# Performance work log

Hardware: AMD Instinct MI355X
Metric: run time of the kernel (lower is better)

The kernel has to match this reference:

```python
import math
import jax, jax.numpy as jnp
import numpy as np

DIM = 1024
N_HEADS = 16
HEAD_DIM = DIM // N_HEADS
MAX_SEQ_LEN = 4096
ROPE_BASE = 10000.0


def _rope_tables(seq_len):
    # [S, head_dim//2] cos/sin tables, matching RotaryPositionalEncoding buffers
    inv_freq = 1.0 / (ROPE_BASE ** (jnp.arange(0, HEAD_DIM, 2, dtype=jnp.float32) / HEAD_DIM))
    t = jnp.arange(seq_len, dtype=jnp.float32)
    freqs = jnp.outer(t, inv_freq)
    return jnp.cos(freqs), jnp.sin(freqs)


def _rotate_half(x):
    # interleaved rotate: out[..., 0::2] = -x[..., 1::2]; out[..., 1::2] = x[..., 0::2]
    x1 = x[..., 0::2]
    x2 = x[..., 1::2]
    return jnp.stack([-x2, x1], axis=-1).reshape(x.shape)


def _apply_rope(xq, xk, cos, sin):
    # cos/sin: [S, head_dim//2] -> repeat_interleave(2) -> [1, 1, S, head_dim]
    cos = jnp.repeat(cos, 2, axis=-1)[None, None]
    sin = jnp.repeat(sin, 2, axis=-1)[None, None]
    xq_out = xq * cos + _rotate_half(xq) * sin
    xk_out = xk * cos + _rotate_half(xk) * sin
    return xq_out, xk_out


def setup_inputs() -> dict:
    key = jax.random.key(0)
    kx, kq, kk, kv, ko = jax.random.split(key, 5)
    B, S = 1, 4096
    x = jax.random.normal(kx, (B, S, DIM), dtype=jnp.float32)
    scale = 0.02
    Wq = jax.random.normal(kq, (DIM, DIM), dtype=jnp.float32) * scale
    Wk = jax.random.normal(kk, (DIM, DIM), dtype=jnp.float32) * scale
    Wv = jax.random.normal(kv, (DIM, DIM), dtype=jnp.float32) * scale
    Wo = jax.random.normal(ko, (DIM, DIM), dtype=jnp.float32) * scale
    return {"x": x, "Wq": Wq, "Wk": Wk, "Wv": Wv, "Wo": Wo}


def reference(x, Wq, Wk, Wv, Wo):
    B, S, _ = x.shape
    # torch nn.Linear: y = x @ W.T
    q = (x @ Wq.T).reshape(B, S, N_HEADS, HEAD_DIM).transpose(0, 2, 1, 3)  # [B,H,S,D]
    k = (x @ Wk.T).reshape(B, S, N_HEADS, HEAD_DIM).transpose(0, 2, 1, 3)
    v = (x @ Wv.T).reshape(B, S, N_HEADS, HEAD_DIM).transpose(0, 2, 1, 3)

    cos, sin = _rope_tables(S)  # start_pos = 0
    q, k = _apply_rope(q, k, cos, sin)

    scores = jnp.einsum('bhqd,bhkd->bhqk', q, k) / math.sqrt(HEAD_DIM)
    # causal mask (start_pos=0, no KV cache): upper triangle above diag gets -inf
    mask = jnp.triu(jnp.full((S, S), -jnp.inf, dtype=scores.dtype), k=1)
    scores = scores + mask[None, None]
    probs = jax.nn.softmax(scores, axis=-1)
    out = jnp.einsum('bhqk,bhkd->bhqd', probs, v)  # [B,H,S,D]
    out = out.transpose(0, 2, 1, 3).reshape(B, S, DIM)
    return out @ Wo.T
```

## Files before the change

kernel.cpp:

```cpp
#include <hip/hip_runtime.h>


typedef __attribute__((ext_vector_type(4))) float f32x4;
typedef __attribute__((ext_vector_type(8))) short short8;
typedef __attribute__((ext_vector_type(2))) unsigned int u32x2;
typedef unsigned short u16;

#define SEQ 4096
#define DIMM 1024
#define NH 16
#define HD 64

__device__ __forceinline__ u16 f2b(float f) {
  unsigned u = __float_as_uint(f);
  u += 0x7FFFu + ((u >> 16) & 1u);
  return (u16)(u >> 16);
}
__device__ __forceinline__ f32x4 mfma16(short8 a, short8 b, f32x4 c) {
  return __builtin_amdgcn_mfma_f32_16x16x32_bf16(a, b, c, 0, 0, 0);
}
#define GLL16(gp, lp)                                                        \
  __builtin_amdgcn_global_load_lds(                                          \
      (const __attribute__((address_space(1))) unsigned int*)(gp),           \
      (__attribute__((address_space(3))) unsigned int*)(lp), 16, 0, 0)

__global__ __launch_bounds__(256) void cvt_all(
    const float* __restrict__ x, const float* __restrict__ wq,
    const float* __restrict__ wk, const float* __restrict__ wv,
    const float* __restrict__ wo,
    u16* __restrict__ xb, u16* __restrict__ wqb, u16* __restrict__ wkb,
    u16* __restrict__ wvb, u16* __restrict__ wob, float2* __restrict__ tab) {
  int i = blockIdx.x * 256 + threadIdx.x;
  if (i < 2097152) {
    const float* src;
    u16* dst;
    int j;
    if (i < 1048576) {
      src = x; dst = xb; j = i;
    } else {
      int t = i - 1048576;
      int wsel = t >> 18;
      j = t & 262143;
      src = (wsel == 0) ? wq : (wsel == 1) ? wk : (wsel == 2) ? wv : wo;
      dst = (wsel == 0) ? wqb : (wsel == 1) ? wkb : (wsel == 2) ? wvb : wob;
    }
    float4 v = ((const float4*)src)[j];
    ushort4 o;
    o.x = f2b(v.x); o.y = f2b(v.y); o.z = f2b(v.z); o.w = f2b(v.w);
    ((ushort4*)dst)[j] = o;
  } else {
    int j = i - 2097152;
    int s = j >> 6, d = j & 63, fi = d >> 1;
    float ang = (float)s * powf(10000.0f, -(float)fi * (1.0f / 32.0f));
    float sn, cs;
    sincosf(ang, &sn, &cs);
    tab[j] = make_float2(cs, (d & 1) ? sn : -sn);
  }
}

__global__ __launch_bounds__(256) void gemm_qkv(
    const u16* __restrict__ A, const u16* __restrict__ B,
    const float2* __restrict__ tab, u16* __restrict__ Qh, u16* __restrict__ Kh,
    u16* __restrict__ Vh) {
  const int K = DIMM;
  __shared__ __align__(16) u16 As[2][4096];
  __shared__ __align__(16) u16 Bs[2][4096];
  const int tid = threadIdx.x;
  const int bm = blockIdx.x, bn = blockIdx.y;
  const int w = tid >> 6, lane = tid & 63;
  const int wm = w >> 1, wn = w & 1;
  const int l15 = lane & 15, g = lane >> 4;

  f32x4 acc[4][4] = {};

  const u16* Ap0 = A + (size_t)(bm * 128 + (tid >> 2)) * K + (tid & 3) * 8;
  const u16* Ap1 = Ap0 + (size_t)64 * K;
  const u16* Bp0 = B + (size_t)(bn * 128 + (tid >> 2)) * K + (tid & 3) * 8;
  const u16* Bp1 = Bp0 + (size_t)64 * K;

  GLL16(Ap0, &As[0][w * 512]);
  GLL16(Ap1, &As[0][2048 + w * 512]);
  GLL16(Bp0, &Bs[0][w * 512]);
  GLL16(Bp1, &Bs[0][2048 + w * 512]);
  __syncthreads();

  const int nk = K >> 5;
  for (int t = 0; t < nk; ++t) {
    const int cur = t & 1;
    if (t + 1 < nk) {
      const int k1 = (t + 1) * 32;
      GLL16(Ap0 + k1, &As[cur ^ 1][w * 512]);
      GLL16(Ap1 + k1, &As[cur ^ 1][2048 + w * 512]);
      GLL16(Bp0 + k1, &Bs[cur ^ 1][w * 512]);
      GLL16(Bp1 + k1, &Bs[cur ^ 1][2048 + w * 512]);
    }
    short8 af[4], bf[4];
#pragma unroll
    for (int m = 0; m < 4; ++m)
      af[m] = *(const short8*)&As[cur][(wm * 64 + m * 16 + l15) * 32 + g * 8];
#pragma unroll
    for (int n = 0; n < 4; ++n)
      bf[n] = *(const short8*)&Bs[cur][(wn * 64 + n * 16 + l15) * 32 + g * 8];
#pragma unroll
    for (int m = 0; m < 4; ++m)
#pragma unroll
      for (int n = 0; n < 4; ++n)
        acc[m][n] = mfma16(af[m], bf[n], acc[m][n]);
    __syncthreads();
  }

  const int sector = bn >> 3;
  const int hh = (bn & 7) * 2 + wn;
  u16* dst = (sector == 0) ? Qh : (sector == 1) ? Kh : Vh;
  const float qs = (sector == 0) ? 0.125f : 1.0f;
  const int evenlane = !(l15 & 1);
  const int dd0 = (l15 & ~1);
#pragma unroll
  for (int m = 0; m < 4; ++m) {
    const int sb = bm * 128 + wm * 64 + m * 16 + g * 4;
#pragma unroll
    for (int n = 0; n < 4; ++n) {
      const int d = n * 16 + l15;
      float val[4];
#pragma unroll
      for (int r = 0; r < 4; ++r) {
        float v = acc[m][n][r];
        if (sector < 2) {
          float p = __shfl_xor(v, 1);
          float2 tc = tab[(sb + r) * 64 + d];
          val[r] = (v * tc.x + p * tc.y) * qs;
        } else {
          val[r] = v;
        }
      }
      float x0 = __shfl_xor(val[0], 1);
      float x1 = __shfl_xor(val[1], 1);
      float x2 = __shfl_xor(val[2], 1);
      float x3 = __shfl_xor(val[3], 1);
      float aLo = evenlane ? val[0] : x2;
      float aHi = evenlane ? x0 : val[2];
      float bLo = evenlane ? val[1] : x3;
      float bHi = evenlane ? x1 : val[3];
      unsigned pkA, pkB;
      asm("v_cvt_pk_bf16_f32 %0, %1, %2" : "=v"(pkA) : "v"(aLo), "v"(aHi));
      asm("v_cvt_pk_bf16_f32 %0, %1, %2" : "=v"(pkB) : "v"(bLo), "v"(bHi));
      const int rA = evenlane ? 0 : 2, rB = evenlane ? 1 : 3;
      const int dcol = n * 16 + dd0;
      *(unsigned*)&dst[((size_t)hh * SEQ + sb + rA) * HD + dcol] = pkA;
      *(unsigned*)&dst[((size_t)hh * SEQ + sb + rB) * HD + dcol] = pkB;
    }
  }
}

__global__ __launch_bounds__(256) void gemm_o(
    const u16* __restrict__ A, const u16* __restrict__ B, float* __restrict__ C) {
  const int K = DIMM;
  __shared__ __align__(16) u16 As[2][4096];
  __shared__ __align__(16) u16 Bs[2][2048];
  const int tid = threadIdx.x;
  const int bm = blockIdx.x, bn = blockIdx.y;
  const int w = tid >> 6, lane = tid & 63;
  const int wm = w >> 1, wn = w & 1;
  const int l15 = lane & 15, g = lane >> 4;

  f32x4 acc[4][2] = {};

  const u16* Ap0 = A + (size_t)(bm * 128 + (tid >> 2)) * K + (tid & 3) * 8;
  const u16* Ap1 = Ap0 + (size_t)64 * K;
  const u16* Bp0 = B + (size_t)(bn * 64 + (tid >> 2)) * K + (tid & 3) * 8;

  GLL16(Ap0, &As[0][w * 512]);
  GLL16(Ap1, &As[0][2048 + w * 512]);
  GLL16(Bp0, &Bs[0][w * 512]);
  __syncthreads();

  const int nk = K >> 5;
  for (int t = 0; t < nk; ++t) {
    const int cur = t & 1;
    if (t + 1 < nk) {
      const int k1 = (t + 1) * 32;
      GLL16(Ap0 + k1, &As[cur ^ 1][w * 512]);
      GLL16(Ap1 + k1, &As[cur ^ 1][2048 + w * 512]);
      GLL16(Bp0 + k1, &Bs[cur ^ 1][w * 512]);
    }
    short8 af[4], bf[2];
#pragma unroll
    for (int m = 0; m < 4; ++m)
      af[m] = *(const short8*)&As[cur][(wm * 64 + m * 16 + l15) * 32 + g * 8];
#pragma unroll
    for (int n = 0; n < 2; ++n)
      bf[n] = *(const short8*)&Bs[cur][(wn * 32 + n * 16 + l15) * 32 + g * 8];
#pragma unroll
    for (int m = 0; m < 4; ++m)
#pragma unroll
      for (int n = 0; n < 2; ++n)
        acc[m][n] = mfma16(af[m], bf[n], acc[m][n]);
    __syncthreads();
  }

#pragma unroll
  for (int m = 0; m < 4; ++m) {
    int grow = bm * 128 + wm * 64 + m * 16 + g * 4;
#pragma unroll
    for (int n = 0; n < 2; ++n) {
      int gcol = bn * 64 + wn * 32 + n * 16 + l15;
#pragma unroll
      for (int r = 0; r < 4; ++r)
        C[(size_t)(grow + r) * DIMM + gcol] = acc[m][n][r];
    }
  }
}

__global__ __launch_bounds__(256, 4) void attn_fwd(
    const u16* __restrict__ Qh, const u16* __restrict__ Kh,
    const u16* __restrict__ Vh, u16* __restrict__ Ob,
    float* __restrict__ Opart, float2* __restrict__ ml) {
  __shared__ __align__(16) u16 Ks[2][64 * 64];
  __shared__ __align__(16) u16 Vt[2][64 * 64];
  __shared__ __align__(16) u16 Ps[4][16 * 64];

  const int L = blockIdx.x;
  const int h = L & 15;
  const int u = L >> 4;
  int c, t0, t1, half = 0;
  if (u < 80) {
    int i = u / 5, j = u % 5;
    if (j < 4) {
      c = 63 - 2 * i - (j >> 1);
      half = j & 1;
      int mid = (c + 2) >> 1;
      t0 = half ? mid : 0;
      t1 = half ? (c + 1) : mid;
    } else {
      c = 31 - i; t0 = 0; t1 = c + 1;
    }
  } else {
    c = 15 - (u - 80); t0 = 0; t1 = c + 1;
  }
  const int heavy = (c >= 32);
  const int nt = t1 - t0;

  const int tid = threadIdx.x, w = tid >> 6, lane = tid & 63;
  const int l15 = lane & 15, g = lane >> 4;
  const int qr0 = c * 64 + w * 16;
  const size_t hS = (size_t)h * SEQ;

  const int krow0 = w * 8 + (lane >> 3);
  const int kc0 = ((lane & 7) ^ (krow0 & 7)) * 8;
  const int krow1 = 32 + krow0;
  const int kc1 = ((lane & 7) ^ (krow1 & 7)) * 8;
  const int kvp = tid >> 3, d0 = (tid & 7) * 8;
  const u16* Vsrc = Vh + (hS + kvp * 2) * HD + d0;
  int voff[8];
#pragma unroll
  for (int j = 0; j < 8; ++j) {
    int d = d0 + j;
    int sw = (d ^ (d >> 3)) & 7;
    voff[j] = d * 64 + (((kvp >> 2) ^ sw) << 3) + (kvp & 3) * 2;
  }

  const u16* Qp = Qh + (hS + qr0 + l15) * HD + g * 8;
  short8 qf0 = *(const short8*)(Qp);
  short8 qf1 = *(const short8*)(Qp + 32);

  f32x4 o[4] = {};
  float m_ = -3.0e38f, lg = 0.f;

  GLL16(Kh + (hS + (size_t)t0 * 64 + krow0) * HD + kc0, &Ks[0][w * 512]);
  GLL16(Kh + (hS + (size_t)t0 * 64 + krow1) * HD + kc1, &Ks[0][2048 + w * 512]);
  short8 va = *(const short8*)(Vsrc + (size_t)t0 * 64 * HD);
  short8 vb = *(const short8*)(Vsrc + (size_t)t0 * 64 * HD + HD);

  for (int tt = 0; tt < nt; ++tt) {
    const int t = t0 + tt;
    const int cur = tt & 1;
    {
      u16* vtb = &Vt[cur][0];
#pragma unroll
      for (int j = 0; j < 8; ++j) {
        ushort2 pr;
        pr.x = (u16)va[j];
        pr.y = (u16)vb[j];
        *(ushort2*)(vtb + voff[j]) = pr;
      }
    }
    __syncthreads();
    if (tt + 1 < nt) {
      const size_t kb_ = hS + (size_t)(t + 1) * 64;
      GLL16(Kh + (kb_ + krow0) * HD + kc0, &Ks[cur ^ 1][w * 512]);
      GLL16(Kh + (kb_ + krow1) * HD + kc1, &Ks[cur ^ 1][2048 + w * 512]);
      va = *(const short8*)(Vsrc + (size_t)(t + 1) * 64 * HD);
      vb = *(const short8*)(Vsrc + (size_t)(t + 1) * 64 * HD + HD);
    }
    f32x4 s[4] = {};
    __builtin_amdgcn_s_setprio(1);
#pragma unroll
    for (int kb = 0; kb < 4; ++kb) {
      int row = kb * 16 + l15;
      short8 k0 = *(const short8*)&Ks[cur][row * 64 + ((g ^ (row & 7)) << 3)];
      short8 k1 = *(const short8*)&Ks[cur][row * 64 + (((4 + g) ^ (row & 7)) << 3)];
      s[kb] = mfma16(k0, qf0, s[kb]);
      s[kb] = mfma16(k1, qf1, s[kb]);
    }
    __builtin_amdgcn_s_setprio(0);
    if (t == c) {
      const int kv0 = t * 64;
      int q = qr0 + l15;
#pragma unroll
      for (int kb = 0; kb < 4; ++kb) {
        int kvb = kv0 + kb * 16 + g * 4;
#pragma unroll
        for (int r = 0; r < 4; ++r)
          if (kvb + r > q) s[kb][r] = -1.0e30f;
      }
    }
    float mx = fmaxf(fmaxf(fmaxf(s[0][0], s[0][1]), fmaxf(s[0][2], s[0][3])),
                     fmaxf(fmaxf(fmaxf(s[1][0], s[1][1]), fmaxf(s[1][2], s[1][3])),
                           fmaxf(fmaxf(fmaxf(s[2][0], s[2][1]), fmaxf(s[2][2], s[2][3])),
                                 fmaxf(fmaxf(s[3][0], s[3][1]), fmaxf(s[3][2], s[3][3])))));
    mx = fmaxf(mx, __shfl_xor(mx, 16));
    mx = fmaxf(mx, __shfl_xor(mx, 32));
    if (!__all(mx - m_ <= 8.0f)) {
      float nm = fmaxf(m_, mx);
      float sc = __expf(m_ - nm);
      m_ = nm;
      lg *= sc;
#pragma unroll
      for (int r = 0; r < 4; ++r) {
        float so = __shfl(sc, g * 4 + r);
        o[0][r] *= so; o[1][r] *= so; o[2][r] *= so; o[3][r] *= so;
      }
    }
    {
      float ps = 0.f;
#pragma unroll
      for (int kb = 0; kb < 4; ++kb) {
        float p0 = __expf(s[kb][0] - m_);
        float p1 = __expf(s[kb][1] - m_);
        float p2 = __expf(s[kb][2] - m_);
        float p3 = __expf(s[kb][3] - m_);
        ps += (p0 + p1) + (p2 + p3);
        unsigned w0, w1;
        asm("v_cvt_pk_bf16_f32 %0, %1, %2" : "=v"(w0) : "v"(p0), "v"(p1));
        asm("v_cvt_pk_bf16_f32 %0, %1, %2" : "=v"(w1) : "v"(p2), "v"(p3));
        int ch = (kb * 2 + (g >> 1)) ^ (l15 & 7);
        *(u32x2*)&Ps[w][l15 * 64 + ch * 8 + (g & 1) * 4] = (u32x2){w0, w1};
      }
      lg += ps;
    }
    short8 pa0 = *(const short8*)&Ps[w][l15 * 64 + ((g ^ (l15 & 7)) << 3)];
    short8 pa1 = *(const short8*)&Ps[w][l15 * 64 + (((4 + g) ^ (l15 & 7)) << 3)];
    __builtin_amdgcn_s_setprio(1);
#pragma unroll
    for (int nb = 0; nb < 4; ++nb) {
      int rv = nb * 16 + l15;
      int swv = (rv ^ (rv >> 3)) & 7;
      short8 v0f = *(const short8*)&Vt[cur][rv * 64 + ((g ^ swv) << 3)];
      short8 v1f = *(const short8*)&Vt[cur][rv * 64 + (((4 + g) ^ swv) << 3)];
      o[nb] = mfma16(pa0, v0f, o[nb]);
      o[nb] = mfma16(pa1, v1f, o[nb]);
    }
    __builtin_amdgcn_s_setprio(0);
  }

  float l = lg;
  l += __shfl_xor(l, 16);
  l += __shfl_xor(l, 32);
  if (heavy) {
    const int p = (h * 32 + (c - 32)) * 2 + half;
    if (lane < 16)
      ml[p * 64 + w * 16 + l15] = make_float2(m_, l);
    float* Od = Opart + ((size_t)p << 12);
#pragma unroll
    for (int nb = 0; nb < 4; ++nb)
#pragma unroll
      for (int r = 0; r < 4; ++r)
        Od[(w * 16 + g * 4 + r) * 64 + nb * 16 + l15] = o[nb][r];
  } else {
    float il = 1.0f / l;
#pragma unroll
    for (int r = 0; r < 4; ++r) {
      float ilr = __shfl(il, g * 4 + r);
      int qrow = qr0 + g * 4 + r;
#pragma unroll
      for (int nb = 0; nb < 4; ++nb)
        Ob[(size_t)qrow * DIMM + h * HD + nb * 16 + l15] = f2b(o[nb][r] * ilr);
    }
  }
}

__global__ __launch_bounds__(256) void attn_merge(
    const float* __restrict__ Opart, const float2* __restrict__ ml,
    u16* __restrict__ Ob) {
  const int slot = blockIdx.x;
  const int h = slot >> 5;
  const int c = 32 + (slot & 31);
  const int t = threadIdx.x;
  const int q = t >> 2, dq = (t & 3) << 4;
  const int pA = slot * 2, pB = pA + 1;
  float2 a = ml[pA * 64 + q], b = ml[pB * 64 + q];
  float m = fmaxf(a.x, b.x);
  float fA = __expf(a.x - m), fB = __expf(b.x - m);
  float il = 1.0f / (a.y * fA + b.y * fB);
  const float* OA = Opart + ((size_t)pA << 12) + q * 64 + dq;
  const float* OB = Opart + ((size_t)pB << 12) + q * 64 + dq;
  u16* dst = Ob + (size_t)(c * 64 + q) * DIMM + h * HD + dq;
#pragma unroll
  for (int jj = 0; jj < 16; jj += 4) {
    float4 va = *(const float4*)(OA + jj);
    float4 vb = *(const float4*)(OB + jj);
    ushort4 o4;
    o4.x = f2b((va.x * fA + vb.x * fB) * il);
    o4.y = f2b((va.y * fA + vb.y * fB) * il);
    o4.z = f2b((va.z * fA + vb.z * fB) * il);
    o4.w = f2b((va.w * fA + vb.w * fB) * il);
    *(ushort4*)(dst + jj) = o4;
  }
}

#define OFF_XB 0u
#define OFF_WQKV 8388608u
#define OFF_WOB 14680064u
#define OFF_TAB 16777216u
#define OFF_QH 18874368u
#define OFF_KH 27262976u
#define OFF_VH 35651584u
#define OFF_OB 44040192u
#define OFF_OPART 52428800u
#define OFF_ML 69206016u

extern "C" void kernel_launch(void* const* d_in, const int* in_sizes, int n_in,
                              void* d_out, int out_size, void* d_ws, size_t ws_size,
                              hipStream_t stream) {
  const float* x = (const float*)d_in[0];
  const float* Wq = (const float*)d_in[1];
  const float* Wk = (const float*)d_in[2];
  const float* Wv = (const float*)d_in[3];
  const float* Wo = (const float*)d_in[4];
  float* out = (float*)d_out;
  char* ws = (char*)d_ws;

  u16* xb = (u16*)(ws + OFF_XB);
  u16* wqkv = (u16*)(ws + OFF_WQKV);
  u16* wqb = wqkv;
  u16* wkb = wqkv + (size_t)DIMM * DIMM;
  u16* wvb = wqkv + (size_t)2 * DIMM * DIMM;
  u16* wob = (u16*)(ws + OFF_WOB);
  float2* tab = (float2*)(ws + OFF_TAB);
  u16* Qh = (u16*)(ws + OFF_QH);
  u16* Kh = (u16*)(ws + OFF_KH);
  u16* Vh = (u16*)(ws + OFF_VH);
  u16* Ob = (u16*)(ws + OFF_OB);
  float* Opart = (float*)(ws + OFF_OPART);
  float2* ml = (float2*)(ws + OFF_ML);

  cvt_all<<<9216, 256, 0, stream>>>(x, Wq, Wk, Wv, Wo, xb, wqb, wkb, wvb, wob, tab);

  gemm_qkv<<<dim3(32, 24), 256, 0, stream>>>(xb, wqkv, tab, Qh, Kh, Vh);

  attn_fwd<<<1536, 256, 0, stream>>>(Qh, Kh, Vh, Ob, Opart, ml);

  attn_merge<<<512, 256, 0, stream>>>(Opart, ml, Ob);

  gemm_o<<<dim3(32, 16), 256, 0, stream>>>(Ob, wob, out);
}
```

Measured before the change: 231.0 us.

## Pre-transpose V into a separate buffer and swizzle GEMM LDS tiles

Result: no change. 234.1 us (+1.3%).

```diff
diff --git a/kernel.cpp b/kernel.cpp
--- a/kernel.cpp
+++ b/kernel.cpp
@@ -73,9 +73,11 @@
 
   f32x4 acc[4][4] = {};
 
-  const u16* Ap0 = A + (size_t)(bm * 128 + (tid >> 2)) * K + (tid & 3) * 8;
+  const int arow = tid >> 2;
+  const int acol = ((tid & 3) ^ ((arow >> 1) & 3)) * 8;
+  const u16* Ap0 = A + (size_t)(bm * 128 + arow) * K + acol;
   const u16* Ap1 = Ap0 + (size_t)64 * K;
-  const u16* Bp0 = B + (size_t)(bn * 128 + (tid >> 2)) * K + (tid & 3) * 8;
+  const u16* Bp0 = B + (size_t)(bn * 128 + arow) * K + acol;
   const u16* Bp1 = Bp0 + (size_t)64 * K;
 
   GLL16(Ap0, &As[0][w * 512]);
@@ -84,6 +86,8 @@
   GLL16(Bp1, &Bs[0][2048 + w * 512]);
   __syncthreads();
 
+  const int kx = (l15 >> 1) & 3;
+  const int c0 = (g ^ kx) << 3;
   const int nk = K >> 5;
   for (int t = 0; t < nk; ++t) {
     const int cur = t & 1;
@@ -97,10 +101,10 @@
     short8 af[4], bf[4];
 #pragma unroll
     for (int m = 0; m < 4; ++m)
-      af[m] = *(const short8*)&As[cur][(wm * 64 + m * 16 + l15) * 32 + g * 8];
+      af[m] = *(const short8*)&As[cur][(wm * 64 + m * 16 + l15) * 32 + c0];
 #pragma unroll
     for (int n = 0; n < 4; ++n)
-      bf[n] = *(const short8*)&Bs[cur][(wn * 64 + n * 16 + l15) * 32 + g * 8];
+      bf[n] = *(const short8*)&Bs[cur][(wn * 64 + n * 16 + l15) * 32 + c0];
 #pragma unroll
     for (int m = 0; m < 4; ++m)
 #pragma unroll
@@ -152,6 +156,31 @@
   }
 }
 
+__global__ __launch_bounds__(256) void vtrans(
+    const u16* __restrict__ Vh, u16* __restrict__ VhT) {
+  __shared__ u16 T[64][72];
+  const int b = blockIdx.x;
+  const int h = b >> 6, s0 = (b & 63) * 64;
+  const int tid = threadIdx.x;
+  const int r = tid >> 3, c8 = (tid & 7) * 8;
+#pragma unroll
+  for (int rep = 0; rep < 2; ++rep) {
+    const int row = rep * 32 + r;
+    *(short8*)&T[row][c8] =
+        *(const short8*)&Vh[((size_t)h * SEQ + s0 + row) * HD + c8];
+  }
+  __syncthreads();
+  const int d = tid >> 2;
+#pragma unroll
+  for (int rep = 0; rep < 2; ++rep) {
+    const int ss = (tid & 3) * 8 + rep * 32;
+    short8 v;
+#pragma unroll
+    for (int j = 0; j < 8; ++j) v[j] = T[ss + j][d];
+    *(short8*)&VhT[((size_t)h * HD + d) * SEQ + s0 + ss] = v;
+  }
+}
+
 __global__ __launch_bounds__(256) void gemm_o(
     const u16* __restrict__ A, const u16* __restrict__ B, float* __restrict__ C) {
   const int K = DIMM;
@@ -165,15 +194,19 @@
 
   f32x4 acc[4][2] = {};
 
-  const u16* Ap0 = A + (size_t)(bm * 128 + (tid >> 2)) * K + (tid & 3) * 8;
+  const int arow = tid >> 2;
+  const int acol = ((tid & 3) ^ ((arow >> 1) & 3)) * 8;
+  const u16* Ap0 = A + (size_t)(bm * 128 + arow) * K + acol;
   const u16* Ap1 = Ap0 + (size_t)64 * K;
-  const u16* Bp0 = B + (size_t)(bn * 64 + (tid >> 2)) * K + (tid & 3) * 8;
+  const u16* Bp0 = B + (size_t)(bn * 64 + arow) * K + acol;
 
   GLL16(Ap0, &As[0][w * 512]);
   GLL16(Ap1, &As[0][2048 + w * 512]);
   GLL16(Bp0, &Bs[0][w * 512]);
   __syncthreads();
 
+  const int kx = (l15 >> 1) & 3;
+  const int c0 = (g ^ kx) << 3;
   const int nk = K >> 5;
   for (int t = 0; t < nk; ++t) {
     const int cur = t & 1;
@@ -186,10 +219,10 @@
     short8 af[4], bf[2];
 #pragma unroll
     for (int m = 0; m < 4; ++m)
-      af[m] = *(const short8*)&As[cur][(wm * 64 + m * 16 + l15) * 32 + g * 8];
+      af[m] = *(const short8*)&As[cur][(wm * 64 + m * 16 + l15) * 32 + c0];
 #pragma unroll
     for (int n = 0; n < 2; ++n)
-      bf[n] = *(const short8*)&Bs[cur][(wn * 32 + n * 16 + l15) * 32 + g * 8];
+      bf[n] = *(const short8*)&Bs[cur][(wn * 32 + n * 16 + l15) * 32 + c0];
 #pragma unroll
     for (int m = 0; m < 4; ++m)
 #pragma unroll
@@ -213,7 +246,7 @@
 
 __global__ __launch_bounds__(256, 4) void attn_fwd(
     const u16* __restrict__ Qh, const u16* __restrict__ Kh,
-    const u16* __restrict__ Vh, u16* __restrict__ Ob,
+    const u16* __restrict__ VhT, u16* __restrict__ Ob,
     float* __restrict__ Opart, float2* __restrict__ ml) {
   __shared__ __align__(16) u16 Ks[2][64 * 64];
   __shared__ __align__(16) u16 Vt[2][64 * 64];
@@ -244,20 +277,12 @@
   const int l15 = lane & 15, g = lane >> 4;
   const int qr0 = c * 64 + w * 16;
   const size_t hS = (size_t)h * SEQ;
+  const size_t hD = (size_t)h * HD;
 
   const int krow0 = w * 8 + (lane >> 3);
   const int kc0 = ((lane & 7) ^ (krow0 & 7)) * 8;
   const int krow1 = 32 + krow0;
   const int kc1 = ((lane & 7) ^ (krow1 & 7)) * 8;
-  const int kvp = tid >> 3, d0 = (tid & 7) * 8;
-  const u16* Vsrc = Vh + (hS + kvp * 2) * HD + d0;
-  int voff[8];
-#pragma unroll
-  for (int j = 0; j < 8; ++j) {
-    int d = d0 + j;
-    int sw = (d ^ (d >> 3)) & 7;
-    voff[j] = d * 64 + (((kvp >> 2) ^ sw) << 3) + (kvp & 3) * 2;
-  }
 
   const u16* Qp = Qh + (hS + qr0 + l15) * HD + g * 8;
   short8 qf0 = *(const short8*)(Qp);
@@ -266,31 +291,24 @@
   f32x4 o[4] = {};
   float m_ = -3.0e38f, lg = 0.f;
 
-  GLL16(Kh + (hS + (size_t)t0 * 64 + krow0) * HD + kc0, &Ks[0][w * 512]);
-  GLL16(Kh + (hS + (size_t)t0 * 64 + krow1) * HD + kc1, &Ks[0][2048 + w * 512]);
-  short8 va = *(const short8*)(Vsrc + (size_t)t0 * 64 * HD);
-  short8 vb = *(const short8*)(Vsrc + (size_t)t0 * 64 * HD + HD);
+  {
+    const int kv0 = t0 * 64;
+    GLL16(Kh + (hS + kv0 + krow0) * HD + kc0, &Ks[0][w * 512]);
+    GLL16(Kh + (hS + kv0 + krow1) * HD + kc1, &Ks[0][2048 + w * 512]);
+    GLL16(VhT + (hD + krow0) * SEQ + kv0 + kc0, &Vt[0][w * 512]);
+    GLL16(VhT + (hD + krow1) * SEQ + kv0 + kc1, &Vt[0][2048 + w * 512]);
+  }
 
   for (int tt = 0; tt < nt; ++tt) {
     const int t = t0 + tt;
     const int cur = tt & 1;
-    {
-      u16* vtb = &Vt[cur][0];
-#pragma unroll
-      for (int j = 0; j < 8; ++j) {
-        ushort2 pr;
-        pr.x = (u16)va[j];
-        pr.y = (u16)vb[j];
-        *(ushort2*)(vtb + voff[j]) = pr;
-      }
-    }
     __syncthreads();
     if (tt + 1 < nt) {
-      const size_t kb_ = hS + (size_t)(t + 1) * 64;
-      GLL16(Kh + (kb_ + krow0) * HD + kc0, &Ks[cur ^ 1][w * 512]);
-      GLL16(Kh + (kb_ + krow1) * HD + kc1, &Ks[cur ^ 1][2048 + w * 512]);
-      va = *(const short8*)(Vsrc + (size_t)(t + 1) * 64 * HD);
-      vb = *(const short8*)(Vsrc + (size_t)(t + 1) * 64 * HD + HD);
+      const int kvn = (t + 1) * 64;
+      GLL16(Kh + (hS + kvn + krow0) * HD + kc0, &Ks[cur ^ 1][w * 512]);
+      GLL16(Kh + (hS + kvn + krow1) * HD + kc1, &Ks[cur ^ 1][2048 + w * 512]);
+      GLL16(VhT + (hD + krow0) * SEQ + kvn + kc0, &Vt[cur ^ 1][w * 512]);
+      GLL16(VhT + (hD + krow1) * SEQ + kvn + kc1, &Vt[cur ^ 1][2048 + w * 512]);
     }
     f32x4 s[4] = {};
     __builtin_amdgcn_s_setprio(1);
@@ -354,9 +372,8 @@
 #pragma unroll
     for (int nb = 0; nb < 4; ++nb) {
       int rv = nb * 16 + l15;
-      int swv = (rv ^ (rv >> 3)) & 7;
-      short8 v0f = *(const short8*)&Vt[cur][rv * 64 + ((g ^ swv) << 3)];
-      short8 v1f = *(const short8*)&Vt[cur][rv * 64 + (((4 + g) ^ swv) << 3)];
+      short8 v0f = *(const short8*)&Vt[cur][rv * 64 + ((g ^ (rv & 7)) << 3)];
+      short8 v1f = *(const short8*)&Vt[cur][rv * 64 + (((4 + g) ^ (rv & 7)) << 3)];
       o[nb] = mfma16(pa0, v0f, o[nb]);
       o[nb] = mfma16(pa1, v1f, o[nb]);
     }
@@ -428,6 +445,7 @@
 #define OFF_OB 44040192u
 #define OFF_OPART 52428800u
 #define OFF_ML 69206016u
+#define OFF_VHT 69730304u
 
 extern "C" void kernel_launch(void* const* d_in, const int* in_sizes, int n_in,
                               void* d_out, int out_size, void* d_ws, size_t ws_size,
@@ -453,12 +471,15 @@
   u16* Ob = (u16*)(ws + OFF_OB);
   float* Opart = (float*)(ws + OFF_OPART);
   float2* ml = (float2*)(ws + OFF_ML);
+  u16* VhT = (u16*)(ws + OFF_VHT);
 
   cvt_all<<<9216, 256, 0, stream>>>(x, Wq, Wk, Wv, Wo, xb, wqb, wkb, wvb, wob, tab);
 
   gemm_qkv<<<dim3(32, 24), 256, 0, stream>>>(xb, wqkv, tab, Qh, Kh, Vh);
 
-  attn_fwd<<<1536, 256, 0, stream>>>(Qh, Kh, Vh, Ob, Opart, ml);
+  vtrans<<<1024, 256, 0, stream>>>(Vh, VhT);
+
+  attn_fwd<<<1536, 256, 0, stream>>>(Qh, Kh, VhT, Ob, Opart, ml);
 
   attn_merge<<<512, 256, 0, stream>>>(Opart, ml, Ob);
 
```
